# Performance work log

Hardware: AMD Instinct MI355X
Metric: run time of the kernel (lower is better)

## Reference

```python
import jax, jax.numpy as jnp
import numpy as np

B, T, L = 32, 256, 784          # batch, decode steps, context length (H*W)
H, E, V = 512, 256, 8000        # decoder hidden, embedding dim, vocab


def setup_inputs() -> dict:
    key = jax.random.key(0)
    ks = jax.random.split(key, 8)
    s = 0.02
    return {
        "cnn_feats": jax.random.normal(ks[0], (B, L, H), jnp.float32),
        "seq": jax.random.randint(ks[1], (B, T), 0, V),
        "embed_w": jax.random.normal(ks[2], (V, E), jnp.float32) * s,
        "w_ih": jax.random.normal(ks[3], (4 * H, E + H), jnp.float32) * s,
        "w_hh": jax.random.normal(ks[4], (4 * H, H), jnp.float32) * s,
        "w_hm": jax.random.normal(ks[5], (H, H), jnp.float32) * s,
        "w_out": jax.random.normal(ks[6], (H, 2 * H), jnp.float32) * s,
        "w_logit": jax.random.normal(ks[7], (V, H), jnp.float32) * s,
        "b_logit": jnp.zeros((V,), jnp.float32),
    }


def reference(cnn_feats, seq, embed_w, w_ih, w_hh, w_hm, w_out, w_logit, b_logit):
    # embed = Embedding -> ReLU (dropout is identity in eval / p=0)
    xs = jax.nn.relu(embed_w[seq])                      # [B, T, E]
    z = jnp.zeros((B, H), cnn_feats.dtype)

    def step(carry, xt):
        h, c, ctx_out = carry
        # LSTMCell (bias=False), input = concat([xt, prev context_output])
        inp = jnp.concatenate([xt, ctx_out], axis=-1)   # [B, E+H]
        gates = inp @ w_ih.T + h @ w_hh.T               # [B, 4H]
        i, f, g, o = jnp.split(gates, 4, axis=-1)       # torch gate order i,f,g,o
        c = jax.nn.sigmoid(f) * c + jax.nn.sigmoid(i) * jnp.tanh(g)
        h = jax.nn.sigmoid(o) * jnp.tanh(c)
        # dot-product attention over context
        mapped = h @ w_hm.T                             # [B, H]
        attn = jax.nn.softmax(jnp.einsum('blh,bh->bl', cnn_feats, mapped), axis=-1)
        ctx = jnp.einsum('bl,blh->bh', attn, cnn_feats)  # [B, H]
        out = jnp.tanh(jnp.concatenate([ctx, h], axis=-1) @ w_out.T)  # [B, H]
        logp = jax.nn.log_softmax(out @ w_logit.T + b_logit, axis=-1)  # [B, V]
        return (h, c, out), logp

    _, logps = jax.lax.scan(step, (z, z, z), jnp.swapaxes(xs, 0, 1))
    return jnp.swapaxes(logps, 0, 1)                    # [B, T, V]
```

## Files before the change

kernel.cpp:

```cpp
#include <hip/hip_runtime.h>
#include <hip/hip_bf16.h>
#include <stdint.h>

typedef unsigned short u16;
typedef unsigned int u32;
typedef unsigned long long u64;
typedef __attribute__((ext_vector_type(8))) short s16x8;
typedef __attribute__((ext_vector_type(4))) float f32x4;

#define AGT __HIP_MEMORY_SCOPE_AGENT

static __device__ __forceinline__ float bf2f(u16 u){
  unsigned v = ((unsigned)u) << 16; return __builtin_bit_cast(float, v);
}
static __device__ __forceinline__ u16 f2bf(float f){
  unsigned u = __builtin_bit_cast(unsigned, f);
  u += 0x7FFFu + ((u >> 16) & 1u);
  return (u16)(u >> 16);
}
static __device__ __forceinline__ float sigm(float x){ return 1.f / (1.f + __expf(-x)); }

typedef __attribute__((address_space(1))) const u32 gu32;
typedef __attribute__((address_space(3))) u32 lu32;
static __device__ __forceinline__ void gload_lds16(const void* g, void* l){
  __builtin_amdgcn_global_load_lds((gu32*)g, (lu32*)l, 16, 0, 0);
}

static __device__ __forceinline__ u64 tload(const u64* p){
  return __hip_atomic_load(p, __ATOMIC_RELAXED, AGT);
}
static __device__ __forceinline__ void tstore(u64* p, u64 v){
  __hip_atomic_store(p, v, __ATOMIC_RELAXED, AGT);
}
static __device__ __forceinline__ u32 wtag(u64 v){ return (u32)(v >> 32); }
static __device__ __forceinline__ s16x8 pack4(u64 q0, u64 q1, u64 q2, u64 q3){
  u32 a0=(u32)q0, a1=(u32)q1, a2=(u32)q2, a3=(u32)q3;
  s16x8 r = {(short)a0,(short)(a0>>16),(short)a1,(short)(a1>>16),
             (short)a2,(short)(a2>>16),(short)a3,(short)(a3>>16)};
  return r;
}


__global__ __launch_bounds__(256) void k_wfull(const float* __restrict__ wih,
                                               const float* __restrict__ whh,
                                               u16* __restrict__ wf){
  int stride = gridDim.x * blockDim.x;
  for (int i = blockIdx.x * blockDim.x + threadIdx.x; i < 2048 * 1280; i += stride){
    int j = i / 1280, k = i - j * 1280;
    float v = (k < 768) ? wih[j * 768 + k] : whh[j * 512 + (k - 768)];
    wf[i] = f2bf(v);
  }
}

__global__ __launch_bounds__(256) void k_whmt(const float* __restrict__ whm,
                                              u16* __restrict__ wt){
  int stride = gridDim.x * blockDim.x;
  for (int i = blockIdx.x * blockDim.x + threadIdx.x; i < 512 * 512; i += stride){
    int n = i >> 9, k = i & 511;
    wt[i] = f2bf(whm[k * 512 + n]);
  }
}

__global__ __launch_bounds__(256) void k_cvt(const float* __restrict__ s,
                                             u16* __restrict__ d, int n){
  int stride = gridDim.x * blockDim.x * 4;
  for (int i = (blockIdx.x * blockDim.x + threadIdx.x) * 4; i < n; i += stride){
    float4 v = *(const float4*)&s[i];
    d[i + 0] = f2bf(v.x); d[i + 1] = f2bf(v.y);
    d[i + 2] = f2bf(v.z); d[i + 3] = f2bf(v.w);
  }
}

__global__ __launch_bounds__(256) void k_xs(const int* __restrict__ seq,
                                            const float* __restrict__ emb,
                                            u16* __restrict__ xs){
  int stride = gridDim.x * blockDim.x;
  for (int i = blockIdx.x * blockDim.x + threadIdx.x; i < 8192 * 256; i += stride){
    int m = i >> 8, e = i & 255;
    int b = m >> 8, t = m & 255;
    float v = emb[(size_t)seq[m] * 256 + e];
    xs[(size_t)(t * 32 + b) * 256 + e] = f2bf(v > 0.f ? v : 0.f);
  }
}


template<int OUTBF, int HASBIAS, int NG>
__global__ __launch_bounds__(256) void k_gemm(const u16* __restrict__ A,
                                              const u16* __restrict__ Bm,
                                              void* __restrict__ Cout,
                                              const float* __restrict__ bias,
                                              int M, int N, int K){
  __shared__ __align__(16) u16 As[128 * 64];
  __shared__ __align__(16) u16 Bs[128 * 64];
  int tid = threadIdx.x; int w = tid >> 6; int l = tid & 63;
  int m0 = blockIdx.x * 128, n0 = blockIdx.y * 128;
  int wr = w >> 1, wc = w & 1;
  f32x4 acc[4][4];
#pragma unroll
  for (int a = 0; a < 4; a++)
#pragma unroll
    for (int b = 0; b < 4; b++){ f32x4 z = {0.f,0.f,0.f,0.f}; acc[a][b] = z; }
  int rA = m0 + (tid >> 3);
  int rB = n0 + (tid >> 3);
  for (int k0 = 0; k0 < K; k0 += 64){
    __syncthreads();
    int ca = k0 + (tid & 7) * 8;
#pragma unroll
    for (int i = 0; i < 4; i++){
      gload_lds16(&A[(size_t)(rA + i * 32) * K + ca], &As[i * 2048 + w * 512]);
      int rb = rB + i * 32;
      if (NG) rb = (rb < N - 1) ? rb : (N - 1);
      gload_lds16(&Bm[(size_t)rb * K + ca], &Bs[i * 2048 + w * 512]);
    }
    asm volatile("s_waitcnt vmcnt(0)" ::: "memory");
    __syncthreads();
#pragma unroll
    for (int ks = 0; ks < 2; ks++){
      s16x8 av[4], bv[4];
      int ko = ks * 32 + (l >> 4) * 8;
#pragma unroll
      for (int i = 0; i < 4; i++) av[i] = *(const s16x8*)&As[(wr * 64 + i * 16 + (l & 15)) * 64 + ko];
#pragma unroll
      for (int i = 0; i < 4; i++) bv[i] = *(const s16x8*)&Bs[(wc * 64 + i * 16 + (l & 15)) * 64 + ko];
#pragma unroll
      for (int mi = 0; mi < 4; mi++)
#pragma unroll
        for (int ni = 0; ni < 4; ni++)
          acc[mi][ni] = __builtin_amdgcn_mfma_f32_16x16x32_bf16(av[mi], bv[ni], acc[mi][ni], 0, 0, 0);
    }
  }
#pragma unroll
  for (int mi = 0; mi < 4; mi++)
#pragma unroll
    for (int ni = 0; ni < 4; ni++){
      int row = m0 + wr * 64 + mi * 16 + (l >> 4) * 4;
      int col = n0 + wc * 64 + ni * 16 + (l & 15);
      if (NG && col >= N) continue;
#pragma unroll
      for (int r = 0; r < 4; r++){
        float v = acc[mi][ni][r];
        if (HASBIAS) v += bias[col];
        if (OUTBF) ((u16*)Cout)[(size_t)(row + r) * N + col] = f2bf(v);
        else       ((float*)Cout)[(size_t)(row + r) * N + col] = v;
      }
    }
}


static __device__ void gates_role(const u16* __restrict__ WF, const u16* __restrict__ XS,
                                  u64* __restrict__ ZH, u64* __restrict__ ZO,
                                  float* __restrict__ CST, float* __restrict__ SM, int g){
  const int tid = threadIdx.x, w = tid >> 6, l = tid & 63;
  const int ns = g << 4;
  float (*red)[32][64] = (float(*)[32][64])SM;

  s16x8 bx[2][4], bh[4][4], bo[4][4];
#pragma unroll
  for (int ki = 0; ki < 2; ki++){
    int ko = w * 64 + ki * 32 + (l >> 4) * 8;
#pragma unroll
    for (int gi = 0; gi < 4; gi++)
      bx[ki][gi] = *(const s16x8*)&WF[(size_t)(gi * 512 + ns + (l & 15)) * 1280 + ko];
  }
#pragma unroll
  for (int ki = 0; ki < 4; ki++){
    int koh = 768 + w * 128 + ki * 32 + (l >> 4) * 8;
    int koo = 256 + w * 128 + ki * 32 + (l >> 4) * 8;
#pragma unroll
    for (int gi = 0; gi < 4; gi++){
      bh[ki][gi] = *(const s16x8*)&WF[(size_t)(gi * 512 + ns + (l & 15)) * 1280 + koh];
      bo[ki][gi] = *(const s16x8*)&WF[(size_t)(gi * 512 + ns + (l & 15)) * 1280 + koo];
    }
  }

  for (int t = 0; t < 256; ++t){
    const u32 tg = (u32)t;
    const int rp = (t + 1) & 1;
    f32x4 acc[2][4];
#pragma unroll
    for (int a = 0; a < 2; a++)
#pragma unroll
      for (int b = 0; b < 4; b++){ f32x4 z = {0.f,0.f,0.f,0.f}; acc[a][b] = z; }

#pragma unroll
    for (int ki = 0; ki < 2; ki++){
      int ko = w * 64 + ki * 32 + (l >> 4) * 8;
      s16x8 av[2];
#pragma unroll
      for (int mi = 0; mi < 2; mi++)
        av[mi] = *(const s16x8*)&XS[(size_t)(t * 32 + mi * 16 + (l & 15)) * 256 + ko];
#pragma unroll
      for (int mi = 0; mi < 2; mi++)
#pragma unroll
        for (int gi = 0; gi < 4; gi++)
          acc[mi][gi] = __builtin_amdgcn_mfma_f32_16x16x32_bf16(av[mi], bx[ki][gi], acc[mi][gi], 0, 0, 0);
    }
    if (t > 0){
#pragma unroll
      for (int kk = 0; kk < 4; kk++){
        int wb = w * 64 + kk * 16 + ((l >> 4) << 2);
        const u64* p0 = &ZH[(size_t)rp * 8192 + (size_t)(l & 15) * 256 + wb];
        const u64* p1 = &ZH[(size_t)rp * 8192 + (size_t)(16 + (l & 15)) * 256 + wb];
        u64 qa0,qa1,qa2,qa3,qb0,qb1,qb2,qb3; bool ok;
        do {
          qa0=tload(p0); qa1=tload(p0+1); qa2=tload(p0+2); qa3=tload(p0+3);
          qb0=tload(p1); qb1=tload(p1+1); qb2=tload(p1+2); qb3=tload(p1+3);
          ok = (wtag(qa0)==tg)&(wtag(qa1)==tg)&(wtag(qa2)==tg)&(wtag(qa3)==tg)
             & (wtag(qb0)==tg)&(wtag(qb1)==tg)&(wtag(qb2)==tg)&(wtag(qb3)==tg);
          if (!ok) __builtin_amdgcn_s_sleep(1);
        } while (!__all(ok));
        s16x8 av0 = pack4(qa0,qa1,qa2,qa3), av1 = pack4(qb0,qb1,qb2,qb3);
#pragma unroll
        for (int gi = 0; gi < 4; gi++){
          acc[0][gi] = __builtin_amdgcn_mfma_f32_16x16x32_bf16(av0, bh[kk][gi], acc[0][gi], 0, 0, 0);
          acc[1][gi] = __builtin_amdgcn_mfma_f32_16x16x32_bf16(av1, bh[kk][gi], acc[1][gi], 0, 0, 0);
        }
      }
#pragma unroll
      for (int kk = 0; kk < 4; kk++){
        int wb = w * 64 + kk * 16 + ((l >> 4) << 2);
        const u64* p0 = &ZO[(size_t)rp * 8192 + (size_t)(l & 15) * 256 + wb];
        const u64* p1 = &ZO[(size_t)rp * 8192 + (size_t)(16 + (l & 15)) * 256 + wb];
        u64 qa0,qa1,qa2,qa3,qb0,qb1,qb2,qb3; bool ok;
        do {
          qa0=tload(p0); qa1=tload(p0+1); qa2=tload(p0+2); qa3=tload(p0+3);
          qb0=tload(p1); qb1=tload(p1+1); qb2=tload(p1+2); qb3=tload(p1+3);
          ok = (wtag(qa0)==tg)&(wtag(qa1)==tg)&(wtag(qa2)==tg)&(wtag(qa3)==tg)
             & (wtag(qb0)==tg)&(wtag(qb1)==tg)&(wtag(qb2)==tg)&(wtag(qb3)==tg);
          if (!ok) __builtin_amdgcn_s_sleep(1);
        } while (!__all(ok));
        s16x8 av0 = pack4(qa0,qa1,qa2,qa3), av1 = pack4(qb0,qb1,qb2,qb3);
#pragma unroll
        for (int gi = 0; gi < 4; gi++){
          acc[0][gi] = __builtin_amdgcn_mfma_f32_16x16x32_bf16(av0, bo[kk][gi], acc[0][gi], 0, 0, 0);
          acc[1][gi] = __builtin_amdgcn_mfma_f32_16x16x32_bf16(av1, bo[kk][gi], acc[1][gi], 0, 0, 0);
        }
      }
    }
#pragma unroll
    for (int mi = 0; mi < 2; mi++)
#pragma unroll
      for (int gi = 0; gi < 4; gi++)
#pragma unroll
        for (int r = 0; r < 4; r++)
          red[w][mi * 16 + (l >> 4) * 4 + r][gi * 16 + (l & 15)] = acc[mi][gi][r];
    __syncthreads();
    {
      int bi = tid >> 3, j = (tid & 7) * 2;
      float iv0=0,fv0=0,gv0=0,ov0=0, iv1=0,fv1=0,gv1=0,ov1=0;
#pragma unroll
      for (int qq = 0; qq < 4; qq++){
        iv0 += red[qq][bi][j];      fv0 += red[qq][bi][16 + j];
        gv0 += red[qq][bi][32 + j]; ov0 += red[qq][bi][48 + j];
        iv1 += red[qq][bi][j + 1];      fv1 += red[qq][bi][16 + j + 1];
        gv1 += red[qq][bi][32 + j + 1]; ov1 += red[qq][bi][48 + j + 1];
      }
      int n0 = ns + j;
      float c0 = (t > 0) ? CST[bi * 512 + n0]     : 0.f;
      float c1 = (t > 0) ? CST[bi * 512 + n0 + 1] : 0.f;
      float cn0 = sigm(fv0) * c0 + sigm(iv0) * tanhf(gv0);
      float cn1 = sigm(fv1) * c1 + sigm(iv1) * tanhf(gv1);
      float h0 = sigm(ov0) * tanhf(cn0);
      float h1 = sigm(ov1) * tanhf(cn1);
      CST[bi * 512 + n0] = cn0; CST[bi * 512 + n0 + 1] = cn1;
      u32 pk = (u32)f2bf(h0) | ((u32)f2bf(h1) << 16);
      tstore(&ZH[(size_t)(t & 1) * 8192 + (size_t)bi * 256 + g * 8 + (tid & 7)],
             ((u64)(u32)(t + 1) << 32) | pk);
    }
    __syncthreads();
  }
}


static __device__ void attn_role(const u16* __restrict__ CNN2, const u16* __restrict__ CNNB,
                                 const u16* __restrict__ WOUT,
                                 u64* __restrict__ ZH, u64* __restrict__ ZO,
                                 u64* __restrict__ UT, u64* __restrict__ MST,
                                 u16* __restrict__ OALL, float* __restrict__ SM, int q){
  const int tid = threadIdx.x, w = tid >> 6, l = tid & 63;
  const int b = q / 7, ch = q - b * 7;
  const int l0 = ch * 112;
  const int nc = (ch == 6) ? 68 : 74, cs = ch * 74;
  u16*   hsh  = (u16*)SM;
  u16*   pbf  = (u16*)(SM + 256);
  float* scp  = SM + 320;
  float* msh  = SM + 768;
  u32*   zsh  = (u32*)(SM + 784);
  float* opart= SM + 1040;

  s16x8 a2[7][4];
  s16x8 vb[8][4];
#pragma unroll
  for (int tile = 0; tile < 7; tile++)
#pragma unroll
    for (int kk = 0; kk < 4; kk++)
      a2[tile][kk] = *(const s16x8*)&CNN2[(size_t)(b * 784 + l0 + tile * 16 + (l & 15)) * 512
                                          + w * 128 + kk * 32 + (l >> 4) * 8];
#pragma unroll
  for (int nt = 0; nt < 8; nt++)
#pragma unroll
    for (int kk = 0; kk < 4; kk++){
      int col = w * 128 + nt * 16 + (l & 15);
#pragma unroll
      for (int j = 0; j < 8; j++){
        int krow = kk * 32 + (l >> 4) * 8 + j;
        vb[nt][kk][j] = (krow < 112)
          ? (short)CNNB[(size_t)(b * 784 + l0 + krow) * 512 + col] : (short)0;
      }
    }

  for (int t = 0; t < 256; ++t){
    const u32 tagp = (u32)(t + 1);
    {
      const u64* hp = &ZH[(size_t)(t & 1) * 8192 + (size_t)b * 256 + tid];
      u64 hw; bool ok;
      do {
        hw = tload(hp);
        ok = (wtag(hw) == tagp);
        if (!ok) __builtin_amdgcn_s_sleep(1);
      } while (!__all(ok));
      ((u32*)hsh)[tid] = (u32)hw;
    }
    __syncthreads();

    f32x4 sac[7];
#pragma unroll
    for (int tile = 0; tile < 7; tile++){ f32x4 z = {0.f,0.f,0.f,0.f}; sac[tile] = z; }
#pragma unroll
    for (int kk = 0; kk < 4; kk++){
      s16x8 bv = *(const s16x8*)&hsh[w * 128 + kk * 32 + (l >> 4) * 8];
#pragma unroll
      for (int tile = 0; tile < 7; tile++)
        sac[tile] = __builtin_amdgcn_mfma_f32_16x16x32_bf16(a2[tile][kk], bv, sac[tile], 0, 0, 0);
    }
    if ((l & 15) == 0){
#pragma unroll
      for (int tile = 0; tile < 7; tile++)
#pragma unroll
        for (int r = 0; r < 4; r++)
          scp[w * 112 + tile * 16 + (l >> 4) * 4 + r] = sac[tile][r];
    }
    __syncthreads();

    float v0 = scp[l] + scp[112 + l] + scp[224 + l] + scp[336 + l];
    float v64 = (l < 48) ? (scp[64 + l] + scp[176 + l] + scp[288 + l] + scp[400 + l]) : -1e30f;
    float m2 = fmaxf(v0, v64);
#pragma unroll
    for (int mk = 1; mk < 64; mk <<= 1) m2 = fmaxf(m2, __shfl_xor(m2, mk, 64));
    float M = m2;
    float p0 = __expf(v0 - M);
    float p64 = (l < 48) ? __expf(v64 - M) : 0.f;
    if (w == 0){ pbf[l] = f2bf(p0); pbf[64 + l] = f2bf(p64); }
    float s2 = p0 + p64;
#pragma unroll
    for (int mk = 1; mk < 64; mk <<= 1) s2 += __shfl_xor(s2, mk, 64);
    float S = s2;
    __syncthreads();

    f32x4 uac[8];
#pragma unroll
    for (int nt = 0; nt < 8; nt++){ f32x4 z = {0.f,0.f,0.f,0.f}; uac[nt] = z; }
#pragma unroll
    for (int kk = 0; kk < 4; kk++){
      s16x8 av = *(const s16x8*)&pbf[kk * 32 + (l >> 4) * 8];
#pragma unroll
      for (int nt = 0; nt < 8; nt++)
        uac[nt] = __builtin_amdgcn_mfma_f32_16x16x32_bf16(av, vb[nt][kk], uac[nt], 0, 0, 0);
    }
#pragma unroll
    for (int nt = 0; nt < 8; nt++){
      float o0 = uac[nt][0];
      float o1 = __shfl_xor(o0, 1, 64);
      if (l < 16 && (l & 1) == 0){
        u64 wv = ((u64)tagp << 32) | (u32)f2bf(o0) | ((u32)f2bf(o1) << 16);
        tstore(&UT[((size_t)(b * 7 + ch)) * 256 + w * 64 + nt * 8 + (l >> 1)], wv);
      }
    }
    if (tid == 0){
      tstore(&MST[(b * 7 + ch) * 2 + 0], ((u64)tagp << 32) | __builtin_bit_cast(u32, M));
      tstore(&MST[(b * 7 + ch) * 2 + 1], ((u64)tagp << 32) | __builtin_bit_cast(u32, S));
    }

    f32x4 oac[5];
#pragma unroll
    for (int tile = 0; tile < 5; tile++){ f32x4 z = {0.f,0.f,0.f,0.f}; oac[tile] = z; }
#pragma unroll
    for (int kk = 0; kk < 4; kk++){
      int ko = w * 128 + kk * 32 + (l >> 4) * 8;
      s16x8 bv = *(const s16x8*)&hsh[ko];
#pragma unroll
      for (int tile = 0; tile < 5; tile++){
        int row = cs + tile * 16 + (l & 15);
        row = (row < 511) ? row : 511;
        s16x8 av = *(const s16x8*)&WOUT[(size_t)row * 1024 + 512 + ko];
        oac[tile] = __builtin_amdgcn_mfma_f32_16x16x32_bf16(av, bv, oac[tile], 0, 0, 0);
      }
    }

    u64 uw[7]; u64 msv = 0;
    {
      bool ok;
      do {
#pragma unroll
        for (int c = 0; c < 7; c++) uw[c] = tload(&UT[((size_t)(b * 7 + c)) * 256 + tid]);
        ok = true;
#pragma unroll
        for (int c = 0; c < 7; c++) ok &= (wtag(uw[c]) == tagp);
        if (w == 0){
          msv = tload(&MST[b * 14 + ((l < 14) ? l : 0)]);
          ok &= (wtag(msv) == tagp);
        }
        if (!ok) __builtin_amdgcn_s_sleep(1);
      } while (!__all(ok));
    }
    if (w == 0 && l < 14) msh[l] = __builtin_bit_cast(float, (u32)msv);
    __syncthreads();
    float Mg = -1e30f;
#pragma unroll
    for (int c = 0; c < 7; c++) Mg = fmaxf(Mg, msh[2 * c]);
    float bet[7]; float Sg = 0.f;
#pragma unroll
    for (int c = 0; c < 7; c++){
      float e = __expf(msh[2 * c] - Mg);
      bet[c] = e; Sg += e * msh[2 * c + 1];
    }
    float inv = 1.f / Sg;
    {
      float c0 = 0.f, c1 = 0.f;
#pragma unroll
      for (int c = 0; c < 7; c++){
        float bc = bet[c] * inv;
        c0 = fmaf(bc, bf2f((u16)uw[c]), c0);
        c1 = fmaf(bc, bf2f((u16)(uw[c] >> 16)), c1);
      }
      zsh[tid] = (u32)f2bf(c0) | ((u32)f2bf(c1) << 16);
    }
    __syncthreads();

#pragma unroll
    for (int kk = 0; kk < 4; kk++){
      int ko = w * 128 + kk * 32 + (l >> 4) * 8;
      s16x8 bv = *(const s16x8*)((const u16*)zsh + ko);
#pragma unroll
      for (int tile = 0; tile < 5; tile++){
        int row = cs + tile * 16 + (l & 15);
        row = (row < 511) ? row : 511;
        s16x8 av = *(const s16x8*)&WOUT[(size_t)row * 1024 + ko];
        oac[tile] = __builtin_amdgcn_mfma_f32_16x16x32_bf16(av, bv, oac[tile], 0, 0, 0);
      }
    }
    if ((l & 15) == 0){
#pragma unroll
      for (int tile = 0; tile < 5; tile++)
#pragma unroll
        for (int r = 0; r < 4; r++)
          opart[w * 80 + tile * 16 + (l >> 4) * 4 + r] = oac[tile][r];
    }
    __syncthreads();
    if (tid < (nc >> 1)){
      int j0 = 2 * tid;
      float v0o = opart[j0]   + opart[80 + j0]   + opart[160 + j0]   + opart[240 + j0];
      float v1o = opart[j0+1] + opart[80 + j0+1] + opart[160 + j0+1] + opart[240 + j0+1];
      u32 pk = (u32)f2bf(tanhf(v0o)) | ((u32)f2bf(tanhf(v1o)) << 16);
      tstore(&ZO[(size_t)(t & 1) * 8192 + (size_t)b * 256 + (cs >> 1) + tid],
             ((u64)tagp << 32) | pk);
      *(u32*)&OALL[((size_t)(b * 256 + t)) * 512 + cs + j0] = pk;
    }
    __syncthreads();
  }
}


__global__ __launch_bounds__(256, 1) void k_persist(const u16* __restrict__ WF,
                                                    const u16* __restrict__ XS,
                                                    const u16* __restrict__ CNN2,
                                                    const u16* __restrict__ CNNB,
                                                    const u16* __restrict__ WOUT,
                                                    u64* __restrict__ ZH,
                                                    u64* __restrict__ ZO,
                                                    u64* __restrict__ UT,
                                                    u64* __restrict__ MST,
                                                    float* __restrict__ CST,
                                                    u16* __restrict__ OALL){
  __shared__ __align__(16) float SM[8192];
  int gid = blockIdx.x;
  if (gid < 32)
    gates_role(WF, XS, ZH, ZO, CST, SM, gid);
  else
    attn_role(CNN2, CNNB, WOUT, ZH, ZO, UT, MST, OALL, SM, gid - 32);
}


__global__ __launch_bounds__(256) void k_lsm(float* __restrict__ x){
  size_t base = (size_t)blockIdx.x * 8000;
  int tid = threadIdx.x, w = tid >> 6, ln = tid & 63;
  __shared__ float sm_[4], ss_[4];
  const float4* xv = (const float4*)(x + base);
  float m = -1e30f, s = 0.f;
  for (int v = tid; v < 2000; v += 256){
    float4 f = xv[v];
    float mm = fmaxf(fmaxf(f.x, f.y), fmaxf(f.z, f.w));
    float ss = __expf(f.x-mm)+__expf(f.y-mm)+__expf(f.z-mm)+__expf(f.w-mm);
    float nm = fmaxf(m, mm);
    s = s * __expf(m - nm) + ss * __expf(mm - nm);
    m = nm;
  }
#pragma unroll
  for (int mk = 1; mk < 64; mk <<= 1){
    float mo = __shfl_xor(m, mk, 64), so = __shfl_xor(s, mk, 64);
    float nm = fmaxf(m, mo);
    s = s * __expf(m - nm) + so * __expf(mo - nm);
    m = nm;
  }
  if (ln == 0){ sm_[w] = m; ss_[w] = s; }
  __syncthreads();
  float M = -1e30f, S = 0.f;
#pragma unroll
  for (int q2 = 0; q2 < 4; q2++){
    float mo = sm_[q2], so = ss_[q2];
    float nm = fmaxf(M, mo);
    S = S * __expf(M - nm) + so * __expf(mo - nm);
    M = nm;
  }
  float lz = M + logf(S);
  float4* xw = (float4*)(x + base);
  for (int v = tid; v < 2000; v += 256){
    float4 f = xw[v];
    f.x -= lz; f.y -= lz; f.z -= lz; f.w -= lz;
    xw[v] = f;
  }
}


extern "C" void kernel_launch(void* const* d_in, const int* in_sizes, int n_in,
                              void* d_out, int out_size, void* d_ws, size_t ws_size,
                              hipStream_t stream){
  const float* cnn  = (const float*)d_in[0];
  const int*   seq  = (const int*)d_in[1];
  const float* emb  = (const float*)d_in[2];
  const float* wih  = (const float*)d_in[3];
  const float* whh  = (const float*)d_in[4];
  const float* whm  = (const float*)d_in[5];
  const float* wo   = (const float*)d_in[6];
  const float* wlg  = (const float*)d_in[7];
  const float* blg  = (const float*)d_in[8];

  char* ws = (char*)d_ws;
  u16*   WF     = (u16*)(ws + 0);
  u16*   WHMT   = (u16*)(ws + 5242880);
  u16*   WOUT   = (u16*)(ws + 5767168);
  u16*   WLOGIT = (u16*)(ws + 6815744);
  u16*   CNNBF  = (u16*)(ws + 15007744);
  u16*   CNN2   = (u16*)(ws + 40697856);
  u16*   XS     = (u16*)(ws + 66387968);
  u16*   OALL   = (u16*)(ws + 70582272);
  u64*   ZH     = (u64*)(ws + 78970880);
  u64*   ZO     = (u64*)(ws + 79101952);
  u64*   UT     = (u64*)(ws + 79233024);
  u64*   MST    = (u64*)(ws + 79691776);
  float* CST    = (float*)(ws + 79695360);

  float* OUT = (float*)d_out;

  (void)hipMemsetAsync(ws + 78970880, 0, 724480, stream);
  k_wfull<<<512, 256, 0, stream>>>(wih, whh, WF);
  k_whmt<<<128, 256, 0, stream>>>(whm, WHMT);
  k_cvt<<<512, 256, 0, stream>>>(wo, WOUT, 512 * 1024);
  k_cvt<<<2048, 256, 0, stream>>>(wlg, WLOGIT, 8000 * 512);
  k_cvt<<<2048, 256, 0, stream>>>(cnn, CNNBF, 25088 * 512);
  k_xs<<<2048, 256, 0, stream>>>(seq, emb, XS);

  {
    dim3 g(196, 4);
    k_gemm<1, 0, 0><<<g, 256, 0, stream>>>(CNNBF, WHMT, CNN2, nullptr, 25088, 512, 512);
  }

  k_persist<<<256, 256, 0, stream>>>(WF, XS, CNN2, CNNBF, WOUT, ZH, ZO, UT, MST, CST, OALL);

  {
    dim3 g(64, 63);
    k_gemm<0, 1, 1><<<g, 256, 0, stream>>>(OALL, WLOGIT, OUT, blg, 8192, 8000, 512);
  }
  k_lsm<<<8192, 256, 0, stream>>>(OUT);
}
```

Before: 3.243 ms.

## Fuse prep kernels and compute softmax stats in logit GEMM epilogue

Merges the six weight/input conversion kernels into a single launch that dispatches on block index. It also has the logit GEMM epilogue compute per-row, per-tile max and sum-exp partials and write them to a stats buffer. The log-softmax kernel then combines the 63 partials per row instead of re-reading the full 8000-wide logits row for its reduction. This removes one full read pass over the 262 MB logits output and some launch overhead, at the cost of extra shuffles and syncs in the GEMM epilogue.

```diff
diff --git a/kernel.cpp b/kernel.cpp
--- a/kernel.cpp
+++ b/kernel.cpp
@@ -41,54 +41,64 @@
 }
 
 
-__global__ __launch_bounds__(256) void k_wfull(const float* __restrict__ wih,
-                                               const float* __restrict__ whh,
-                                               u16* __restrict__ wf){
-  int stride = gridDim.x * blockDim.x;
-  for (int i = blockIdx.x * blockDim.x + threadIdx.x; i < 2048 * 1280; i += stride){
-    int j = i / 1280, k = i - j * 1280;
-    float v = (k < 768) ? wih[j * 768 + k] : whh[j * 512 + (k - 768)];
-    wf[i] = f2bf(v);
-  }
-}
-
-__global__ __launch_bounds__(256) void k_whmt(const float* __restrict__ whm,
-                                              u16* __restrict__ wt){
-  int stride = gridDim.x * blockDim.x;
-  for (int i = blockIdx.x * blockDim.x + threadIdx.x; i < 512 * 512; i += stride){
-    int n = i >> 9, k = i & 511;
-    wt[i] = f2bf(whm[k * 512 + n]);
-  }
-}
-
-__global__ __launch_bounds__(256) void k_cvt(const float* __restrict__ s,
-                                             u16* __restrict__ d, int n){
-  int stride = gridDim.x * blockDim.x * 4;
-  for (int i = (blockIdx.x * blockDim.x + threadIdx.x) * 4; i < n; i += stride){
-    float4 v = *(const float4*)&s[i];
-    d[i + 0] = f2bf(v.x); d[i + 1] = f2bf(v.y);
-    d[i + 2] = f2bf(v.z); d[i + 3] = f2bf(v.w);
-  }
-}
-
-__global__ __launch_bounds__(256) void k_xs(const int* __restrict__ seq,
-                                            const float* __restrict__ emb,
-                                            u16* __restrict__ xs){
-  int stride = gridDim.x * blockDim.x;
-  for (int i = blockIdx.x * blockDim.x + threadIdx.x; i < 8192 * 256; i += stride){
-    int m = i >> 8, e = i & 255;
-    int b = m >> 8, t = m & 255;
-    float v = emb[(size_t)seq[m] * 256 + e];
-    xs[(size_t)(t * 32 + b) * 256 + e] = f2bf(v > 0.f ? v : 0.f);
-  }
-}
-
-
-template<int OUTBF, int HASBIAS, int NG>
+__global__ __launch_bounds__(256) void k_prep(const float* __restrict__ wih,
+                                              const float* __restrict__ whh,
+                                              u16* __restrict__ wf,
+                                              const float* __restrict__ whm,
+                                              u16* __restrict__ whmt,
+                                              const float* __restrict__ wo,
+                                              u16* __restrict__ wout,
+                                              const float* __restrict__ wlg,
+                                              u16* __restrict__ wlogit,
+                                              const float* __restrict__ cnn,
+                                              u16* __restrict__ cnnbf,
+                                              const int* __restrict__ seq,
+                                              const float* __restrict__ emb,
+                                              u16* __restrict__ xs){
+  int bid = blockIdx.x, tid = threadIdx.x;
+  if (bid < 512){
+    for (int i = bid * 256 + tid; i < 2048 * 1280; i += 512 * 256){
+      int j = i / 1280, k = i - j * 1280;
+      float v = (k < 768) ? wih[j * 768 + k] : whh[j * 512 + (k - 768)];
+      wf[i] = f2bf(v);
+    }
+  } else if (bid < 640){
+    for (int i = (bid - 512) * 256 + tid; i < 512 * 512; i += 128 * 256){
+      int n = i >> 9, k = i & 511;
+      whmt[i] = f2bf(whm[k * 512 + n]);
+    }
+  } else if (bid < 1152){
+    for (int i = ((bid - 640) * 256 + tid) * 4; i < 512 * 1024; i += 512 * 256 * 4){
+      float4 v = *(const float4*)&wo[i];
+      wout[i+0]=f2bf(v.x); wout[i+1]=f2bf(v.y); wout[i+2]=f2bf(v.z); wout[i+3]=f2bf(v.w);
+    }
+  } else if (bid < 2176){
+    for (int i = ((bid - 1152) * 256 + tid) * 4; i < 8000 * 512; i += 1024 * 256 * 4){
+      float4 v = *(const float4*)&wlg[i];
+      wlogit[i+0]=f2bf(v.x); wlogit[i+1]=f2bf(v.y); wlogit[i+2]=f2bf(v.z); wlogit[i+3]=f2bf(v.w);
+    }
+  } else if (bid < 4224){
+    for (int i = ((bid - 2176) * 256 + tid) * 4; i < 25088 * 512; i += 2048 * 256 * 4){
+      float4 v = *(const float4*)&cnn[i];
+      cnnbf[i+0]=f2bf(v.x); cnnbf[i+1]=f2bf(v.y); cnnbf[i+2]=f2bf(v.z); cnnbf[i+3]=f2bf(v.w);
+    }
+  } else {
+    for (int i = (bid - 4224) * 256 + tid; i < 8192 * 256; i += 2048 * 256){
+      int m = i >> 8, e = i & 255;
+      int b = m >> 8, t = m & 255;
+      float v = emb[(size_t)seq[m] * 256 + e];
+      xs[(size_t)(t * 32 + b) * 256 + e] = f2bf(v > 0.f ? v : 0.f);
+    }
+  }
+}
+
+
+template<int OUTBF, int HASBIAS, int NG, int STATS>
 __global__ __launch_bounds__(256) void k_gemm(const u16* __restrict__ A,
                                               const u16* __restrict__ Bm,
                                               void* __restrict__ Cout,
                                               const float* __restrict__ bias,
+                                              float* __restrict__ stats,
                                               int M, int N, int K){
   __shared__ __align__(16) u16 As[128 * 64];
   __shared__ __align__(16) u16 Bs[128 * 64];
@@ -144,6 +154,47 @@
         else       ((float*)Cout)[(size_t)(row + r) * N + col] = v;
       }
     }
+  if (STATS){
+    __syncthreads();
+    float* st = (float*)As;
+#pragma unroll
+    for (int mi = 0; mi < 4; mi++)
+#pragma unroll
+      for (int r = 0; r < 4; r++){
+        float vv[4]; float mx = -1e30f;
+#pragma unroll
+        for (int ni = 0; ni < 4; ni++){
+          int col = n0 + wc * 64 + ni * 16 + (l & 15);
+          int cb = (NG && col >= N) ? (N - 1) : col;
+          float v = acc[mi][ni][r] + (HASBIAS ? bias[cb] : 0.f);
+          vv[ni] = (NG && col >= N) ? -1e30f : v;
+          mx = fmaxf(mx, vv[ni]);
+        }
+        float sm = 0.f;
+#pragma unroll
+        for (int ni = 0; ni < 4; ni++) sm += (vv[ni] > -1e29f) ? __expf(vv[ni] - mx) : 0.f;
+#pragma unroll
+        for (int mk = 1; mk < 16; mk <<= 1){
+          float mo = __shfl_xor(mx, mk, 64), so = __shfl_xor(sm, mk, 64);
+          float nm = fmaxf(mx, mo);
+          sm = sm * __expf(mx - nm) + so * __expf(mo - nm);
+          mx = nm;
+        }
+        if ((l & 15) == 0){
+          int rr = wr * 64 + mi * 16 + (l >> 4) * 4 + r;
+          st[rr * 4 + wc * 2 + 0] = mx;
+          st[rr * 4 + wc * 2 + 1] = sm;
+        }
+      }
+    __syncthreads();
+    if (tid < 128){
+      float ma = st[tid*4], sa = st[tid*4+1], mb = st[tid*4+2], sb = st[tid*4+3];
+      float nm = fmaxf(ma, mb);
+      float ss = sa * __expf(ma - nm) + sb * __expf(mb - nm);
+      size_t idx = ((size_t)(m0 + tid) * 64 + blockIdx.y) * 2;
+      stats[idx] = nm; stats[idx + 1] = ss;
+    }
+  }
 }
 
 
@@ -491,39 +542,29 @@
 }
 
 
-__global__ __launch_bounds__(256) void k_lsm(float* __restrict__ x){
-  size_t base = (size_t)blockIdx.x * 8000;
+__global__ __launch_bounds__(256) void k_lsm2(float* __restrict__ x,
+                                              const float* __restrict__ stats){
+  size_t row = blockIdx.x;
   int tid = threadIdx.x, w = tid >> 6, ln = tid & 63;
-  __shared__ float sm_[4], ss_[4];
-  const float4* xv = (const float4*)(x + base);
-  float m = -1e30f, s = 0.f;
-  for (int v = tid; v < 2000; v += 256){
-    float4 f = xv[v];
-    float mm = fmaxf(fmaxf(f.x, f.y), fmaxf(f.z, f.w));
-    float ss = __expf(f.x-mm)+__expf(f.y-mm)+__expf(f.z-mm)+__expf(f.w-mm);
-    float nm = fmaxf(m, mm);
-    s = s * __expf(m - nm) + ss * __expf(mm - nm);
-    m = nm;
-  }
-#pragma unroll
-  for (int mk = 1; mk < 64; mk <<= 1){
-    float mo = __shfl_xor(m, mk, 64), so = __shfl_xor(s, mk, 64);
-    float nm = fmaxf(m, mo);
-    s = s * __expf(m - nm) + so * __expf(mo - nm);
-    m = nm;
-  }
-  if (ln == 0){ sm_[w] = m; ss_[w] = s; }
+  __shared__ float lzsh;
+  if (w == 0){
+    float m = -1e30f, s = 0.f;
+    if (ln < 63){
+      m = stats[(row * 64 + ln) * 2];
+      s = stats[(row * 64 + ln) * 2 + 1];
+    }
+#pragma unroll
+    for (int mk = 1; mk < 64; mk <<= 1){
+      float mo = __shfl_xor(m, mk, 64), so = __shfl_xor(s, mk, 64);
+      float nm = fmaxf(m, mo);
+      s = s * __expf(m - nm) + so * __expf(mo - nm);
+      m = nm;
+    }
+    if (ln == 0) lzsh = m + logf(s);
+  }
   __syncthreads();
-  float M = -1e30f, S = 0.f;
-#pragma unroll
-  for (int q2 = 0; q2 < 4; q2++){
-    float mo = sm_[q2], so = ss_[q2];
-    float nm = fmaxf(M, mo);
-    S = S * __expf(M - nm) + so * __expf(mo - nm);
-    M = nm;
-  }
-  float lz = M + logf(S);
-  float4* xw = (float4*)(x + base);
+  float lz = lzsh;
+  float4* xw = (float4*)(x + row * 8000);
   for (int v = tid; v < 2000; v += 256){
     float4 f = xw[v];
     f.x -= lz; f.y -= lz; f.z -= lz; f.w -= lz;
@@ -559,27 +600,24 @@
   u64*   UT     = (u64*)(ws + 79233024);
   u64*   MST    = (u64*)(ws + 79691776);
   float* CST    = (float*)(ws + 79695360);
+  float* STATS  = (float*)(ws + 79760896);
 
   float* OUT = (float*)d_out;
 
   (void)hipMemsetAsync(ws + 78970880, 0, 724480, stream);
-  k_wfull<<<512, 256, 0, stream>>>(wih, whh, WF);
-  k_whmt<<<128, 256, 0, stream>>>(whm, WHMT);
-  k_cvt<<<512, 256, 0, stream>>>(wo, WOUT, 512 * 1024);
-  k_cvt<<<2048, 256, 0, stream>>>(wlg, WLOGIT, 8000 * 512);
-  k_cvt<<<2048, 256, 0, stream>>>(cnn, CNNBF, 25088 * 512);
-  k_xs<<<2048, 256, 0, stream>>>(seq, emb, XS);
+  k_prep<<<6272, 256, 0, stream>>>(wih, whh, WF, whm, WHMT, wo, WOUT,
+                                   wlg, WLOGIT, cnn, CNNBF, seq, emb, XS);
 
   {
     dim3 g(196, 4);
-    k_gemm<1, 0, 0><<<g, 256, 0, stream>>>(CNNBF, WHMT, CNN2, nullptr, 25088, 512, 512);
+    k_gemm<1, 0, 0, 0><<<g, 256, 0, stream>>>(CNNBF, WHMT, CNN2, nullptr, nullptr, 25088, 512, 512);
   }
 
   k_persist<<<256, 256, 0, stream>>>(WF, XS, CNN2, CNNBF, WOUT, ZH, ZO, UT, MST, CST, OALL);
 
   {
     dim3 g(64, 63);
-    k_gemm<0, 1, 1><<<g, 256, 0, stream>>>(OALL, WLOGIT, OUT, blg, 8192, 8000, 512);
-  }
-  k_lsm<<<8192, 256, 0, stream>>>(OUT);
-}
+    k_gemm<0, 1, 1, 1><<<g, 256, 0, stream>>>(OALL, WLOGIT, OUT, blg, STATS, 8192, 8000, 512);
+  }
+  k_lsm2<<<8192, 256, 0, stream>>>(OUT, STATS);
+}
```

Measured after the change: 3.233 ms. Within noise of the previous version (-0.3%).
